# Performance work log

Hardware: AMD Instinct MI355X
Metric: run time of the kernel (lower is better)

## Reference

```python
import jax, jax.numpy as jnp
import numpy as np

Q_DIM = 256
CTX_DIM = 256
FF_DIM = 1024
B, LQ, LKV = 8, 2048, 4096


def setup_inputs() -> dict:
    key = jax.random.key(0)
    ks = jax.random.split(key, 16)
    s = lambda d: 1.0 / np.sqrt(d)
    return {
        "query": jax.random.normal(ks[0], (B, LQ, Q_DIM), jnp.float32),
        "key": jax.random.normal(ks[1], (B, LKV, CTX_DIM), jnp.float32),
        "value": jax.random.normal(ks[2], (B, LKV, CTX_DIM), jnp.float32),
        # attention projections (stored [in, out])
        "Wk": jax.random.normal(ks[3], (CTX_DIM, Q_DIM), jnp.float32) * s(CTX_DIM),
        "bk": jnp.zeros((Q_DIM,), jnp.float32),
        "Wv": jax.random.normal(ks[4], (CTX_DIM, Q_DIM), jnp.float32) * s(CTX_DIM),
        "bv": jnp.zeros((Q_DIM,), jnp.float32),
        "Wo": jax.random.normal(ks[5], (Q_DIM, Q_DIM), jnp.float32) * s(Q_DIM),
        "bo": jnp.zeros((Q_DIM,), jnp.float32),
        # layernorms
        "g1": jnp.ones((Q_DIM,), jnp.float32),
        "b1": jnp.zeros((Q_DIM,), jnp.float32),
        "g2": jnp.ones((Q_DIM,), jnp.float32),
        "b2": jnp.zeros((Q_DIM,), jnp.float32),
        # feedforward
        "W1": jax.random.normal(ks[6], (Q_DIM, FF_DIM), jnp.float32) * s(Q_DIM),
        "bf1": jnp.zeros((FF_DIM,), jnp.float32),
        "W2": jax.random.normal(ks[7], (FF_DIM, Q_DIM), jnp.float32) * s(FF_DIM),
        "bf2": jnp.zeros((Q_DIM,), jnp.float32),
    }


def _layernorm(x, g, b, eps=1e-5):
    mu = jnp.mean(x, axis=-1, keepdims=True)
    var = jnp.var(x, axis=-1, keepdims=True)
    return (x - mu) * jax.lax.rsqrt(var + eps) * g + b


def reference(query, key, value, Wk, bk, Wv, bv, Wo, bo, g1, b1, g2, b2, W1, bf1, W2, bf2):
    # CrossAttention (single-head, naive)
    key_proj = key @ Wk + bk        # [B, Lkv, D]
    value_proj = value @ Wv + bv    # [B, Lkv, D]
    scale = 1.0 / jnp.sqrt(jnp.asarray(Q_DIM, query.dtype))
    scores = jnp.einsum("bqd,bkd->bqk", query, key_proj) * scale  # [B, Lq, Lkv]
    weights = jax.nn.softmax(scores, axis=-1)
    context = jnp.einsum("bqk,bkd->bqd", weights, value_proj)     # [B, Lq, D]
    attn_out = context @ Wo + bo
    # residual + LN
    x = _layernorm(query + attn_out, g1, b1)
    # FeedForward (condition_dim=0, dropout=0)
    ff = jax.nn.relu(x @ W1 + bf1) @ W2 + bf2
    return _layernorm(x + ff, g2, b2)
```

## Files before the change

### kernel.cpp

```cpp
#include <hip/hip_runtime.h>
#include <stdint.h>

typedef __attribute__((ext_vector_type(4))) float f32x4;
typedef __attribute__((ext_vector_type(16))) float f32x16;
typedef __attribute__((ext_vector_type(8))) short short8;
typedef __attribute__((ext_vector_type(4))) short short4v;
typedef __attribute__((ext_vector_type(4))) unsigned uint4v;

__device__ __forceinline__ short f2bf(float f) {
  union { float f; uint32_t u; } v; v.f = f;
  uint32_t r = v.u + 0x7FFFu + ((v.u >> 16) & 1u);
  return (short)(r >> 16);
}

__device__ __forceinline__ float bf2f(short s) {
  union { unsigned u; float f; } v; v.u = ((unsigned)(unsigned short)s) << 16; return v.f;
}

__device__ __forceinline__ unsigned cvt_pk_bf16(float lo, float hi) {
  unsigned r;
  asm("v_cvt_pk_bf16_f32 %0, %1, %2" : "=v"(r) : "v"(lo), "v"(hi));
  return r;
}

__device__ __forceinline__ void pl32swap(unsigned& x, unsigned& y) {
  asm volatile("v_permlane32_swap_b32 %0, %1" : "+v"(x), "+v"(y));
}

__device__ __forceinline__ f32x4 mfma16(short8 a, short8 b, f32x4 c) {
  return __builtin_amdgcn_mfma_f32_16x16x32_bf16(a, b, c, 0, 0, 0);
}
__device__ __forceinline__ f32x16 mfma32(short8 a, short8 b, f32x16 c) {
  return __builtin_amdgcn_mfma_f32_32x32x16_bf16(a, b, c, 0, 0, 0);
}

#define NB 8
#define LQ 2048
#define LKV 4096
#define DQ 256
#define FF 1024
#define NCHUNK 2
#define ROWS (NB * LQ)
#define MFIX 10.0f

#define AS1(p) ((const __attribute__((address_space(1))) void*)(p))
#define AS3(p) ((__attribute__((address_space(3))) void*)(p))

__global__ void transpose_all(
    const float* __restrict__ Wk, const float* __restrict__ Wv,
    const float* __restrict__ Wo, const float* __restrict__ W1,
    const float* __restrict__ W2,
    short* __restrict__ WkT, short* __restrict__ WvT, short* __restrict__ WoT,
    short* __restrict__ W1T, short* __restrict__ W2T) {
  __shared__ float t[32][33];
  int bid = blockIdx.x;
  const float* in; short* out; int R, C, b0;
  if (bid < 64)       { in = Wk; out = WkT; R = 256;  C = 256;  b0 = bid; }
  else if (bid < 128) { in = Wv; out = WvT; R = 256;  C = 256;  b0 = bid - 64; }
  else if (bid < 192) { in = Wo; out = WoT; R = 256;  C = 256;  b0 = bid - 128; }
  else if (bid < 448) { in = W1; out = W1T; R = 256;  C = 1024; b0 = bid - 192; }
  else                { in = W2; out = W2T; R = 1024; C = 256;  b0 = bid - 448; }
  int nbx = C / 32;
  int c0 = (b0 % nbx) * 32, r0 = (b0 / nbx) * 32;
  int tx = threadIdx.x, ty = threadIdx.y;
#pragma unroll
  for (int dy = 0; dy < 32; dy += 8)
    t[ty + dy][tx] = in[(long)(r0 + ty + dy) * C + c0 + tx];
  __syncthreads();
#pragma unroll
  for (int dy = 0; dy < 32; dy += 8)
    out[(long)(c0 + ty + dy) * R + r0 + tx] = f2bf(t[tx][ty + dy]);
}

template <int AMODE, int BMODE, int EPI>
__global__ void __launch_bounds__(256, 2) gemm128(
    const void* __restrict__ A, long sAb, int lda,
    const void* __restrict__ B, long sBb, int ldb,
    const float* __restrict__ bias,
    void* C, long sCb, int ldc, int K) {
  __shared__ char lds[(AMODE == 0 && BMODE == 0) ? 65536 : 32768];
  const int tid = threadIdx.x;
  const int bn = blockIdx.x, bm = blockIdx.y, bz = blockIdx.z;
  const int w = tid >> 6, l = tid & 63;
  const int wm = w & 1, wn = w >> 1;
  const int lr = l & 15, lq = l >> 4;

  auto stageReg = [&](const float* src, int ld, long row0, int k0, char* ldsb) {
#pragma unroll
    for (int it = 0; it < 4; ++it) {
      int idx = it * 2048 + tid * 8;
      int r = idx >> 6, c = idx & 63;
      const float* p = src + (row0 + r) * (long)ld + k0 + c;
      f32x4 f0 = *(const f32x4*)p, f1 = *(const f32x4*)(p + 4);
      uint4v u;
      u[0] = cvt_pk_bf16(f0[0], f0[1]); u[1] = cvt_pk_bf16(f0[2], f0[3]);
      u[2] = cvt_pk_bf16(f1[0], f1[1]); u[3] = cvt_pk_bf16(f1[2], f1[3]);
      *(short8*)(ldsb + ((r * 128 + c * 2) ^ ((r & 7) << 4))) = *(short8*)&u;
    }
  };
  auto stageGld = [&](const short* src, int ld, long row0, int k0, char* ldsb) {
#pragma unroll
    for (int it = 0; it < 4; ++it) {
      const int span = it * 4096 + w * 1024;
      int idx = (span >> 4) + l;
      int r = idx >> 3, c = idx & 7;
      __builtin_amdgcn_global_load_lds(
          AS1(src + (row0 + r) * (long)ld + k0 + ((c ^ (r & 7)) * 8)),
          AS3(ldsb + span), 16, 0, 0);
    }
  };
  auto compute = [&](char* ldsA, char* ldsB, f32x4 (*acc)[4]) {
    short8 af[4][2], bfr[4][2];
#pragma unroll
    for (int i = 0; i < 4; ++i) {
#pragma unroll
      for (int kk = 0; kk < 2; ++kk) {
        int ra = wm * 64 + i * 16 + lr;
        af[i][kk] = *(const short8*)(ldsA + ((ra * 128 + (kk * 32 + lq * 8) * 2) ^ ((ra & 7) << 4)));
        int rb = wn * 64 + i * 16 + lr;
        bfr[i][kk] = *(const short8*)(ldsB + ((rb * 128 + (kk * 32 + lq * 8) * 2) ^ ((rb & 7) << 4)));
      }
    }
#pragma unroll
    for (int i = 0; i < 4; ++i)
#pragma unroll
      for (int j = 0; j < 4; ++j) {
        acc[i][j] = mfma16(af[i][0], bfr[j][0], acc[i][j]);
        acc[i][j] = mfma16(af[i][1], bfr[j][1], acc[i][j]);
      }
  };

  f32x4 acc[4][4] = {};
  if (AMODE == 0 && BMODE == 0) {
    const int NS = K / 64;
    stageGld((const short*)A + sAb * bz, lda, (long)bm * 128, 0, lds);
    stageGld((const short*)B + sBb * bz, ldb, (long)bn * 128, 0, lds + 16384);
    for (int ks = 0; ks < NS; ++ks) {
      if (ks + 1 < NS) {
        char* nbuf = lds + ((ks + 1) & 1) * 32768;
        stageGld((const short*)A + sAb * bz, lda, (long)bm * 128, (ks + 1) * 64, nbuf);
        stageGld((const short*)B + sBb * bz, ldb, (long)bn * 128, (ks + 1) * 64, nbuf + 16384);
        asm volatile("s_waitcnt vmcnt(8)" ::: "memory");
      } else {
        asm volatile("s_waitcnt vmcnt(0)" ::: "memory");
      }
      __builtin_amdgcn_s_barrier();
      __builtin_amdgcn_sched_barrier(0);
      char* buf = lds + (ks & 1) * 32768;
      compute(buf, buf + 16384, acc);
      asm volatile("s_waitcnt lgkmcnt(0)" ::: "memory");
      __builtin_amdgcn_s_barrier();
      __builtin_amdgcn_sched_barrier(0);
    }
  } else {
    for (int k0 = 0; k0 < K; k0 += 64) {
      if (AMODE == 0)      stageGld((const short*)A + sAb * bz, lda, (long)bm * 128, k0, lds);
      else                 stageReg((const float*)A + sAb * bz, lda, (long)bm * 128, k0, lds);
      if (BMODE == 0)      stageGld((const short*)B + sBb * bz, ldb, (long)bn * 128, k0, lds + 16384);
      else                 stageReg((const float*)B + sBb * bz, ldb, (long)bn * 128, k0, lds + 16384);
      __syncthreads();
      compute(lds, lds + 16384, acc);
      __syncthreads();
    }
  }
#pragma unroll
  for (int i = 0; i < 4; ++i) {
#pragma unroll
    for (int j = 0; j < 4; ++j) {
#pragma unroll
      for (int r = 0; r < 4; ++r) {
        long row = (long)bm * 128 + wm * 64 + i * 16 + lq * 4 + r;
        long col = (long)bn * 128 + wn * 64 + j * 16 + lr;
        float v = acc[i][j][r];
        if (EPI == 0) {
          v += bias[col];
          ((short*)C + sCb * bz)[row * ldc + col] = f2bf(v);
        } else if (EPI == 1) {
          v += bias[row];
          ((short*)C + sCb * bz)[row * ldc + col] = f2bf(v);
        } else {
          v += bias[col];
          v = fmaxf(v, 0.f);
          ((short*)C + sCb * bz)[row * ldc + col] = f2bf(v);
        }
      }
    }
  }
}

template <int AMODE, bool RESF32, bool WF32, bool WB16>
__global__ void __launch_bounds__(128, 2) gemmln(
    const void* __restrict__ A, const short* __restrict__ Bw,
    const float* __restrict__ bias, const void* __restrict__ resid,
    const float* __restrict__ Lcomb,
    const float* __restrict__ g, const float* __restrict__ be,
    float* __restrict__ outF, short* __restrict__ outB, int K) {
  __shared__ char lds[(AMODE == 0) ? 73728 : 36864];
  const int tid = threadIdx.x;
  const int bm = blockIdx.x;
  const int w = tid >> 6, l = tid & 63;
  const int lr = l & 15, lq = l >> 4;

  auto stageA0 = [&](int k0, char* ldsA) {
    const short* src = (const short*)A;
#pragma unroll
    for (int it = 0; it < 2; ++it) {
      const int span = it * 2048 + w * 1024;
      int idx = (span >> 4) + l;
      int r = idx >> 3, c = idx & 7;
      __builtin_amdgcn_global_load_lds(
          AS1(src + ((long)bm * 32 + r) * K + k0 + ((c ^ (r & 7)) * 8)),
          AS3(ldsA + span), 16, 0, 0);
    }
  };
  auto stageB = [&](int k0, char* ldsB) {
#pragma unroll
    for (int it = 0; it < 16; ++it) {
      const int span = it * 2048 + w * 1024;
      int idx = (span >> 4) + l;
      int r = idx >> 3, c = idx & 7;
      __builtin_amdgcn_global_load_lds(
          AS1(Bw + (long)r * K + k0 + ((c ^ (r & 7)) * 8)),
          AS3(ldsB + span), 16, 0, 0);
    }
  };
  auto stageA2 = [&](int k0, char* ldsA) {
    const short* O0 = (const short*)A;
#pragma unroll
    for (int it = 0; it < 2; ++it) {
      int idx = it * 1024 + tid * 8;
      int r = idx >> 6, c = idx & 63;
      long row = (long)bm * 32 + r;
      float l0 = Lcomb[row], l1 = Lcomb[ROWS + row];
      float inv = 1.f / (l0 + l1);
      float w0 = l0 * inv, w1 = l1 * inv;
      const short* p0 = O0 + row * 256 + k0 + c;
      short8 v0 = *(const short8*)p0;
      short8 v1 = *(const short8*)(p0 + (long)ROWS * 256);
      uint4v u;
#pragma unroll
      for (int j = 0; j < 4; ++j) {
        float x0 = w0 * bf2f(v0[2 * j])     + w1 * bf2f(v1[2 * j]);
        float x1 = w0 * bf2f(v0[2 * j + 1]) + w1 * bf2f(v1[2 * j + 1]);
        u[j] = cvt_pk_bf16(x0, x1);
      }
      *(short8*)(ldsA + ((r * 128 + c * 2) ^ ((r & 7) << 4))) = *(short8*)&u;
    }
  };

  auto compute = [&](char* ldsA, char* ldsB, f32x4* acc) {
    short8 af0, af1;
    int ra = w * 16 + lr;
    af0 = *(const short8*)(ldsA + ((ra * 128 + (lq * 8) * 2) ^ ((ra & 7) << 4)));
    af1 = *(const short8*)(ldsA + ((ra * 128 + (32 + lq * 8) * 2) ^ ((ra & 7) << 4)));
#pragma unroll
    for (int j = 0; j < 16; ++j) {
      int rb = j * 16 + lr;
      short8 b0 = *(const short8*)(ldsB + ((rb * 128 + (lq * 8) * 2) ^ ((rb & 7) << 4)));
      short8 b1 = *(const short8*)(ldsB + ((rb * 128 + (32 + lq * 8) * 2) ^ ((rb & 7) << 4)));
      acc[j] = mfma16(af0, b0, acc[j]);
      acc[j] = mfma16(af1, b1, acc[j]);
    }
  };

  f32x4 acc[16] = {};
  if (AMODE == 0) {
    const int NS = K / 64;
    stageA0(0, lds);
    stageB(0, lds + 4096);
    for (int ks = 0; ks < NS; ++ks) {
      if (ks + 1 < NS) {
        char* nbuf = lds + ((ks + 1) & 1) * 36864;
        stageA0((ks + 1) * 64, nbuf);
        stageB((ks + 1) * 64, nbuf + 4096);
        asm volatile("s_waitcnt vmcnt(18)" ::: "memory");
      } else {
        asm volatile("s_waitcnt vmcnt(0)" ::: "memory");
      }
      __builtin_amdgcn_s_barrier();
      __builtin_amdgcn_sched_barrier(0);
      char* buf = lds + (ks & 1) * 36864;
      compute(buf, buf + 4096, acc);
      asm volatile("s_waitcnt lgkmcnt(0)" ::: "memory");
      __builtin_amdgcn_s_barrier();
      __builtin_amdgcn_sched_barrier(0);
    }
  } else {
    for (int k0 = 0; k0 < K; k0 += 64) {
      stageA2(k0, lds);
      stageB(k0, lds + 4096);
      __syncthreads();
      compute(lds, lds + 4096, acc);
      __syncthreads();
    }
  }

  const long rowbase = (long)bm * 32 + w * 16;
  float bia[16], gg[16], bb[16];
#pragma unroll
  for (int j = 0; j < 16; ++j) {
    int col = j * 16 + lr;
    bia[j] = bias[col]; gg[j] = g[col]; bb[j] = be[col];
  }
#pragma unroll
  for (int r = 0; r < 4; ++r) {
    long row = rowbase + lq * 4 + r;
    float v[16];
    float s = 0.f, s2 = 0.f;
#pragma unroll
    for (int j = 0; j < 16; ++j) {
      long idx = row * 256 + j * 16 + lr;
      float rx = RESF32 ? ((const float*)resid)[idx] : bf2f(((const short*)resid)[idx]);
      float x = acc[j][r] + bia[j] + rx;
      v[j] = x; s += x; s2 += x * x;
    }
#pragma unroll
    for (int mk = 1; mk < 16; mk <<= 1) { s += __shfl_xor(s, mk); s2 += __shfl_xor(s2, mk); }
    float mu = s * (1.f / 256.f);
    float var = s2 * (1.f / 256.f) - mu * mu;
    float rstd = rsqrtf(var + 1e-5f);
#pragma unroll
    for (int j = 0; j < 16; ++j) {
      int col = j * 16 + lr;
      float y = (v[j] - mu) * rstd * gg[j] + bb[j];
      if (WF32) outF[row * 256 + col] = y;
      if (WB16) outB[row * 256 + col] = f2bf(y);
    }
  }
}

__global__ void __launch_bounds__(256, 1) flash_attn(
    const float* __restrict__ Q, const short* __restrict__ Kb,
    const short* __restrict__ Vt, short* __restrict__ Opart,
    float* __restrict__ Lb) {
  __shared__ char lds[131072];
  const int tid = threadIdx.x;
  const int n = blockIdx.x;
  const int b = n & 7;
  const int slot = n >> 3;
  const int qt = slot & 15;
  const int ch = slot >> 4;
  const int wid = tid >> 6, l = tid & 63;
  const int ql = l & 31, h = l >> 5;
  const int qrow0 = qt * 128 + wid * 32;
  const float* Qp = Q + ((long)b * LQ + qrow0 + ql) * DQ;
  const short* Kp = Kb + (long)b * LKV * DQ;
  const short* Vp = Vt + (long)b * DQ * LKV;
  const float SCQ = 0.0625f * 1.4426950408889634f;

  auto stage = [&](int bufb, int kv0) {
    char* kqb = lds + bufb * 65536;
    char* vtb = kqb + 32768;
#pragma unroll
    for (int i = 0; i < 8; ++i) {
      const int j = wid * 8192 + i * 1024;
      {
        int r = (j >> 9) + (l >> 5);
        int cc = l & 31;
        const short* gk = Kp + (long)(kv0 + r) * DQ + ((cc ^ (r & 15)) * 8);
        __builtin_amdgcn_global_load_lds(AS1(gk), AS3(kqb + j), 16, 0, 0);
      }
      {
        int d = (j >> 7) + (l >> 3);
        int cc = l & 7;
        const short* gv = Vp + (long)d * LKV + kv0 + ((cc ^ (d & 7)) * 8);
        __builtin_amdgcn_global_load_lds(AS1(gv), AS3(vtb + j), 16, 0, 0);
      }
    }
  };

  short8 qf[16];
#pragma unroll
  for (int w = 0; w < 16; ++w) {
    const float* p = Qp + w * 16 + h * 8;
    f32x4 f0 = *(const f32x4*)p, f1 = *(const f32x4*)(p + 4);
    short8 v;
#pragma unroll
    for (int j = 0; j < 4; ++j) { v[j] = f2bf(f0[j] * SCQ); v[4 + j] = f2bf(f1[j] * SCQ); }
    qf[w] = v;
  }

  f32x16 o[8] = {};
  float l_r = 0.f;

  const int kv_lo = ch * (LKV / NCHUNK);
  const int NT = (LKV / NCHUNK) / 64;

  stage(0, kv_lo);

  for (int t = 0; t < NT; ++t) {
    if (t + 1 < NT) {
      stage((t + 1) & 1, kv_lo + (t + 1) * 64);
      asm volatile("s_waitcnt vmcnt(16)" ::: "memory");
    } else {
      asm volatile("s_waitcnt vmcnt(0)" ::: "memory");
    }
    __builtin_amdgcn_s_barrier();
    __builtin_amdgcn_sched_barrier(0);
    char* kq = lds + (t & 1) * 65536;
    char* vt = kq + 32768;

    f32x16 sa = {}, sb = {};
    {
      const int krA = ql, krB = 32 + ql;
      const int baseA = krA * 512, swzA = (krA & 15) << 4;
      const int baseB = krB * 512, swzB = (krB & 15) << 4;
#pragma unroll
      for (int w = 0; w < 16; ++w) {
        short8 kfA = *(const short8*)(kq + ((baseA + w * 32 + h * 16) ^ swzA));
        sa = mfma32(kfA, qf[w], sa);
        short8 kfB = *(const short8*)(kq + ((baseB + w * 32 + h * 16) ^ swzB));
        sb = mfma32(kfB, qf[w], sb);
      }
    }

    short8 paA[2], paB[2];
    float rs0 = 0.f, rs1 = 0.f, rs2 = 0.f, rs3 = 0.f;
    {
      float pA[16];
#pragma unroll
      for (int i = 0; i < 16; ++i) pA[i] = exp2f(sa[i] - MFIX);
#pragma unroll
      for (int i = 0; i < 4; ++i) { rs0 += pA[4 * i]; rs1 += pA[4 * i + 1]; rs2 += pA[4 * i + 2]; rs3 += pA[4 * i + 3]; }
#pragma unroll
      for (int v = 0; v < 2; ++v) {
        unsigned w01 = cvt_pk_bf16(pA[8 * v + 0], pA[8 * v + 1]);
        unsigned w23 = cvt_pk_bf16(pA[8 * v + 2], pA[8 * v + 3]);
        unsigned w45 = cvt_pk_bf16(pA[8 * v + 4], pA[8 * v + 5]);
        unsigned w67 = cvt_pk_bf16(pA[8 * v + 6], pA[8 * v + 7]);
        pl32swap(w01, w45);
        pl32swap(w23, w67);
        uint4v u = {w01, w23, w45, w67};
        paA[v] = *(short8*)&u;
      }
    }
    {
      float pB[16];
#pragma unroll
      for (int i = 0; i < 16; ++i) pB[i] = exp2f(sb[i] - MFIX);
#pragma unroll
      for (int i = 0; i < 4; ++i) { rs0 += pB[4 * i]; rs1 += pB[4 * i + 1]; rs2 += pB[4 * i + 2]; rs3 += pB[4 * i + 3]; }
#pragma unroll
      for (int v = 0; v < 2; ++v) {
        unsigned w01 = cvt_pk_bf16(pB[8 * v + 0], pB[8 * v + 1]);
        unsigned w23 = cvt_pk_bf16(pB[8 * v + 2], pB[8 * v + 3]);
        unsigned w45 = cvt_pk_bf16(pB[8 * v + 4], pB[8 * v + 5]);
        unsigned w67 = cvt_pk_bf16(pB[8 * v + 6], pB[8 * v + 7]);
        pl32swap(w01, w45);
        pl32swap(w23, w67);
        uint4v u = {w01, w23, w45, w67};
        paB[v] = *(short8*)&u;
      }
    }
    {
      float rs = (rs0 + rs1) + (rs2 + rs3);
      rs += __shfl_xor(rs, 32);
      l_r += rs;
    }

#pragma unroll
    for (int nn = 0; nn < 8; ++nn) {
      const int d = 32 * nn + ql;
      const int dbase = d * 128, dswz = (d & 7) << 4;
      short8 bv0 = *(const short8*)(vt + ((dbase + 0 * 32 + 16 * h) ^ dswz));
      o[nn] = mfma32(paA[0], bv0, o[nn]);
      short8 bv1 = *(const short8*)(vt + ((dbase + 1 * 32 + 16 * h) ^ dswz));
      o[nn] = mfma32(paA[1], bv1, o[nn]);
      short8 bv2 = *(const short8*)(vt + ((dbase + 2 * 32 + 16 * h) ^ dswz));
      o[nn] = mfma32(paB[0], bv2, o[nn]);
      short8 bv3 = *(const short8*)(vt + ((dbase + 3 * 32 + 16 * h) ^ dswz));
      o[nn] = mfma32(paB[1], bv3, o[nn]);
    }

    asm volatile("s_waitcnt lgkmcnt(0)" ::: "memory");
    __builtin_amdgcn_s_barrier();
    __builtin_amdgcn_sched_barrier(0);
  }

  const long rowb = (long)b * LQ + qrow0;
  float inv_l = 1.f / l_r;
#pragma unroll
  for (int rr = 0; rr < 16; ++rr) {
    int rloc = (rr & 3) + 8 * (rr >> 2) + 4 * h;
    float li = __shfl(inv_l, rloc + 32 * h);
    long grow = rowb + rloc;
    short* dst = Opart + ((long)ch * ROWS + grow) * 256 + ql;
#pragma unroll
    for (int nn = 0; nn < 8; ++nn) dst[32 * nn] = f2bf(o[nn][rr] * li);
  }
  if (h == 0) {
    Lb[(long)ch * ROWS + rowb + ql] = l_r;
  }
}

extern "C" void kernel_launch(void* const* d_in, const int* in_sizes, int n_in,
                              void* d_out, int out_size, void* d_ws, size_t ws_size,
                              hipStream_t stream) {
  const float* query = (const float*)d_in[0];
  const float* key   = (const float*)d_in[1];
  const float* value = (const float*)d_in[2];
  const float* Wk  = (const float*)d_in[3];
  const float* bk  = (const float*)d_in[4];
  const float* Wv  = (const float*)d_in[5];
  const float* bv  = (const float*)d_in[6];
  const float* Wo  = (const float*)d_in[7];
  const float* bo  = (const float*)d_in[8];
  const float* g1  = (const float*)d_in[9];
  const float* b1  = (const float*)d_in[10];
  const float* g2  = (const float*)d_in[11];
  const float* b2  = (const float*)d_in[12];
  const float* W1  = (const float*)d_in[13];
  const float* bf1 = (const float*)d_in[14];
  const float* W2  = (const float*)d_in[15];
  const float* bf2 = (const float*)d_in[16];

  char* ws = (char*)d_ws;
  size_t off = 0;
  auto take = [&](size_t bytes) { char* p = ws + off; off += bytes; return p; };
  short* WkT = (short*)take((size_t)256 * 256 * 2);
  short* WvT = (short*)take((size_t)256 * 256 * 2);
  short* WoT = (short*)take((size_t)256 * 256 * 2);
  short* W1T = (short*)take((size_t)1024 * 256 * 2);
  short* W2T = (short*)take((size_t)256 * 1024 * 2);
  short* Kb  = (short*)take((size_t)NB * LKV * DQ * 2);
  short* Vt  = (short*)take((size_t)NB * DQ * LKV * 2);
  short* Opart = (short*)take((size_t)NCHUNK * ROWS * 256 * 2);
  float* Lbuf  = (float*)take((size_t)NCHUNK * ROWS * 4);
  short* Xb    = (short*)take((size_t)ROWS * 256 * 2);
  short* Hb  = (short*)Kb;
  (void)ws_size; (void)in_sizes; (void)n_in; (void)out_size;

  dim3 blk(256);
  transpose_all<<<dim3(704), dim3(32, 8), 0, stream>>>(
      Wk, Wv, Wo, W1, W2, WkT, WvT, WoT, W1T, W2T);

  gemm128<1, 0, 0><<<dim3(2, 256, 1), blk, 0, stream>>>(
      key, 0, 256, WkT, 0, 256, bk, Kb, 0, 256, 256);
  gemm128<0, 1, 1><<<dim3(32, 2, 8), blk, 0, stream>>>(
      WvT, 0, 256, value, (long)LKV * 256, 256, bv, Vt, (long)256 * LKV, LKV, 256);
  flash_attn<<<dim3(256), blk, 0, stream>>>(query, Kb, Vt, Opart, Lbuf);
  gemmln<2, true, false, true><<<dim3(ROWS / 32), dim3(128), 0, stream>>>(
      Opart, WoT, bo, query, Lbuf, g1, b1, nullptr, Xb, 256);
  gemm128<0, 0, 3><<<dim3(8, 128, 1), blk, 0, stream>>>(
      Xb, 0, 256, W1T, 0, 256, bf1, Hb, 0, 1024, 256);
  gemmln<0, false, true, false><<<dim3(ROWS / 32), dim3(128), 0, stream>>>(
      Hb, W2T, bf2, Xb, nullptr, g2, b2, (float*)d_out, nullptr, 1024);
}
```

Baseline: 214.6 us.

## Software-pipeline PV matmul one tile behind QK and split K/V staging

```diff
diff --git a/kernel.cpp b/kernel.cpp
--- a/kernel.cpp
+++ b/kernel.cpp
@@ -348,24 +348,26 @@
   const short* Vp = Vt + (long)b * DQ * LKV;
   const float SCQ = 0.0625f * 1.4426950408889634f;
 
-  auto stage = [&](int bufb, int kv0) {
-    char* kqb = lds + bufb * 65536;
-    char* vtb = kqb + 32768;
+  auto stageK = [&](int bufb, int kv0) {
+    char* kqb = lds + bufb * 32768;
 #pragma unroll
     for (int i = 0; i < 8; ++i) {
       const int j = wid * 8192 + i * 1024;
-      {
-        int r = (j >> 9) + (l >> 5);
-        int cc = l & 31;
-        const short* gk = Kp + (long)(kv0 + r) * DQ + ((cc ^ (r & 15)) * 8);
-        __builtin_amdgcn_global_load_lds(AS1(gk), AS3(kqb + j), 16, 0, 0);
-      }
-      {
-        int d = (j >> 7) + (l >> 3);
-        int cc = l & 7;
-        const short* gv = Vp + (long)d * LKV + kv0 + ((cc ^ (d & 7)) * 8);
-        __builtin_amdgcn_global_load_lds(AS1(gv), AS3(vtb + j), 16, 0, 0);
-      }
+      int r = (j >> 9) + (l >> 5);
+      int cc = l & 31;
+      const short* gk = Kp + (long)(kv0 + r) * DQ + ((cc ^ (r & 15)) * 8);
+      __builtin_amdgcn_global_load_lds(AS1(gk), AS3(kqb + j), 16, 0, 0);
+    }
+  };
+  auto stageV = [&](int bufb, int kv0) {
+    char* vtb = lds + 65536 + bufb * 32768;
+#pragma unroll
+    for (int i = 0; i < 8; ++i) {
+      const int j = wid * 8192 + i * 1024;
+      int d = (j >> 7) + (l >> 3);
+      int cc = l & 7;
+      const short* gv = Vp + (long)d * LKV + kv0 + ((cc ^ (d & 7)) * 8);
+      __builtin_amdgcn_global_load_lds(AS1(gv), AS3(vtb + j), 16, 0, 0);
     }
   };
 
@@ -382,23 +384,25 @@
 
   f32x16 o[8] = {};
   float l_r = 0.f;
+  short8 paA[2], paB[2];
 
   const int kv_lo = ch * (LKV / NCHUNK);
   const int NT = (LKV / NCHUNK) / 64;
 
-  stage(0, kv_lo);
+  stageK(0, kv_lo);
+  stageV(0, kv_lo);
 
   for (int t = 0; t < NT; ++t) {
     if (t + 1 < NT) {
-      stage((t + 1) & 1, kv_lo + (t + 1) * 64);
-      asm volatile("s_waitcnt vmcnt(16)" ::: "memory");
+      stageK((t + 1) & 1, kv_lo + (t + 1) * 64);
+      asm volatile("s_waitcnt vmcnt(8)" ::: "memory");
     } else {
       asm volatile("s_waitcnt vmcnt(0)" ::: "memory");
     }
     __builtin_amdgcn_s_barrier();
     __builtin_amdgcn_sched_barrier(0);
-    char* kq = lds + (t & 1) * 65536;
-    char* vt = kq + 32768;
+    char* kq = lds + (t & 1) * 32768;
+    char* vtprev = lds + 65536 + ((t + 1) & 1) * 32768;
 
     f32x16 sa = {}, sb = {};
     {
@@ -414,50 +418,73 @@
       }
     }
 
-    short8 paA[2], paB[2];
-    float rs0 = 0.f, rs1 = 0.f, rs2 = 0.f, rs3 = 0.f;
+    if (t > 0) {
+#pragma unroll
+      for (int nn = 0; nn < 8; ++nn) {
+        const int d = 32 * nn + ql;
+        const int dbase = d * 128, dswz = (d & 7) << 4;
+        short8 bv0 = *(const short8*)(vtprev + ((dbase + 0 * 32 + 16 * h) ^ dswz));
+        o[nn] = mfma32(paA[0], bv0, o[nn]);
+        short8 bv1 = *(const short8*)(vtprev + ((dbase + 1 * 32 + 16 * h) ^ dswz));
+        o[nn] = mfma32(paA[1], bv1, o[nn]);
+        short8 bv2 = *(const short8*)(vtprev + ((dbase + 2 * 32 + 16 * h) ^ dswz));
+        o[nn] = mfma32(paB[0], bv2, o[nn]);
+        short8 bv3 = *(const short8*)(vtprev + ((dbase + 3 * 32 + 16 * h) ^ dswz));
+        o[nn] = mfma32(paB[1], bv3, o[nn]);
+      }
+    }
+
     {
-      float pA[16];
-#pragma unroll
-      for (int i = 0; i < 16; ++i) pA[i] = exp2f(sa[i] - MFIX);
-#pragma unroll
-      for (int i = 0; i < 4; ++i) { rs0 += pA[4 * i]; rs1 += pA[4 * i + 1]; rs2 += pA[4 * i + 2]; rs3 += pA[4 * i + 3]; }
-#pragma unroll
-      for (int v = 0; v < 2; ++v) {
-        unsigned w01 = cvt_pk_bf16(pA[8 * v + 0], pA[8 * v + 1]);
-        unsigned w23 = cvt_pk_bf16(pA[8 * v + 2], pA[8 * v + 3]);
-        unsigned w45 = cvt_pk_bf16(pA[8 * v + 4], pA[8 * v + 5]);
-        unsigned w67 = cvt_pk_bf16(pA[8 * v + 6], pA[8 * v + 7]);
-        pl32swap(w01, w45);
-        pl32swap(w23, w67);
-        uint4v u = {w01, w23, w45, w67};
-        paA[v] = *(short8*)&u;
-      }
-    }
-    {
-      float pB[16];
-#pragma unroll
-      for (int i = 0; i < 16; ++i) pB[i] = exp2f(sb[i] - MFIX);
-#pragma unroll
-      for (int i = 0; i < 4; ++i) { rs0 += pB[4 * i]; rs1 += pB[4 * i + 1]; rs2 += pB[4 * i + 2]; rs3 += pB[4 * i + 3]; }
-#pragma unroll
-      for (int v = 0; v < 2; ++v) {
-        unsigned w01 = cvt_pk_bf16(pB[8 * v + 0], pB[8 * v + 1]);
-        unsigned w23 = cvt_pk_bf16(pB[8 * v + 2], pB[8 * v + 3]);
-        unsigned w45 = cvt_pk_bf16(pB[8 * v + 4], pB[8 * v + 5]);
-        unsigned w67 = cvt_pk_bf16(pB[8 * v + 6], pB[8 * v + 7]);
-        pl32swap(w01, w45);
-        pl32swap(w23, w67);
-        uint4v u = {w01, w23, w45, w67};
-        paB[v] = *(short8*)&u;
-      }
-    }
-    {
+      float rs0 = 0.f, rs1 = 0.f, rs2 = 0.f, rs3 = 0.f;
+      {
+        float pA[16];
+#pragma unroll
+        for (int i = 0; i < 16; ++i) pA[i] = exp2f(sa[i] - MFIX);
+#pragma unroll
+        for (int i = 0; i < 4; ++i) { rs0 += pA[4 * i]; rs1 += pA[4 * i + 1]; rs2 += pA[4 * i + 2]; rs3 += pA[4 * i + 3]; }
+#pragma unroll
+        for (int v = 0; v < 2; ++v) {
+          unsigned w01 = cvt_pk_bf16(pA[8 * v + 0], pA[8 * v + 1]);
+          unsigned w23 = cvt_pk_bf16(pA[8 * v + 2], pA[8 * v + 3]);
+          unsigned w45 = cvt_pk_bf16(pA[8 * v + 4], pA[8 * v + 5]);
+          unsigned w67 = cvt_pk_bf16(pA[8 * v + 6], pA[8 * v + 7]);
+          pl32swap(w01, w45);
+          pl32swap(w23, w67);
+          uint4v u = {w01, w23, w45, w67};
+          paA[v] = *(short8*)&u;
+        }
+      }
+      {
+        float pB[16];
+#pragma unroll
+        for (int i = 0; i < 16; ++i) pB[i] = exp2f(sb[i] - MFIX);
+#pragma unroll
+        for (int i = 0; i < 4; ++i) { rs0 += pB[4 * i]; rs1 += pB[4 * i + 1]; rs2 += pB[4 * i + 2]; rs3 += pB[4 * i + 3]; }
+#pragma unroll
+        for (int v = 0; v < 2; ++v) {
+          unsigned w01 = cvt_pk_bf16(pB[8 * v + 0], pB[8 * v + 1]);
+          unsigned w23 = cvt_pk_bf16(pB[8 * v + 2], pB[8 * v + 3]);
+          unsigned w45 = cvt_pk_bf16(pB[8 * v + 4], pB[8 * v + 5]);
+          unsigned w67 = cvt_pk_bf16(pB[8 * v + 6], pB[8 * v + 7]);
+          pl32swap(w01, w45);
+          pl32swap(w23, w67);
+          uint4v u = {w01, w23, w45, w67};
+          paB[v] = *(short8*)&u;
+        }
+      }
       float rs = (rs0 + rs1) + (rs2 + rs3);
       rs += __shfl_xor(rs, 32);
       l_r += rs;
     }
 
+    asm volatile("s_waitcnt lgkmcnt(0)" ::: "memory");
+    __builtin_amdgcn_s_barrier();
+    __builtin_amdgcn_sched_barrier(0);
+    if (t + 1 < NT) stageV((t + 1) & 1, kv_lo + (t + 1) * 64);
+  }
+
+  {
+    char* vt = lds + 65536 + ((NT - 1) & 1) * 32768;
 #pragma unroll
     for (int nn = 0; nn < 8; ++nn) {
       const int d = 32 * nn + ql;
@@ -471,10 +498,6 @@
       short8 bv3 = *(const short8*)(vt + ((dbase + 3 * 32 + 16 * h) ^ dswz));
       o[nn] = mfma32(paB[1], bv3, o[nn]);
     }
-
-    asm volatile("s_waitcnt lgkmcnt(0)" ::: "memory");
-    __builtin_amdgcn_s_barrier();
-    __builtin_amdgcn_sched_barrier(0);
   }
 
   const long rowb = (long)b * LQ + qrow0;
```

Result: faster. 205.5 us (-4.3%).
